# Kernel optimization log

Measured on AMD Instinct MI355X. Metric: run time of the kernel, lower is better.

Reference implementation:

```python
import jax, jax.numpy as jnp
import numpy as np

HIDDEN = 1024
NUM_HEADS = 16
HEAD_SIZE = HIDDEN // NUM_HEADS


def setup_inputs() -> dict:
    key = jax.random.key(0)
    ks = jax.random.split(key, 5)
    B, S = 2, 2048
    x = jax.random.normal(ks[0], (B, S, HIDDEN), dtype=jnp.float32)
    # nn.Linear(hidden, 3*hidden): weight stored (in, out) for x @ W
    scale_qkv = 1.0 / np.sqrt(HIDDEN)
    w_qkv = jax.random.uniform(ks[1], (HIDDEN, 3 * HIDDEN), minval=-scale_qkv, maxval=scale_qkv, dtype=jnp.float32)
    b_qkv = jax.random.uniform(ks[2], (3 * HIDDEN,), minval=-scale_qkv, maxval=scale_qkv, dtype=jnp.float32)
    w_o = jax.random.uniform(ks[3], (HIDDEN, HIDDEN), minval=-scale_qkv, maxval=scale_qkv, dtype=jnp.float32)
    b_o = jax.random.uniform(ks[4], (HIDDEN,), minval=-scale_qkv, maxval=scale_qkv, dtype=jnp.float32)
    return {"x": x, "w_qkv": w_qkv, "b_qkv": b_qkv, "w_o": w_o, "b_o": b_o}


def reference(x, w_qkv, b_qkv, w_o, b_o):
    B, S, H = x.shape
    qkv = x @ w_qkv + b_qkv  # (B, S, 3H)
    q, k, v = jnp.split(qkv, 3, axis=-1)
    # (B, S, H) -> (B, nheads, S, head_size)
    def heads(t):
        return t.reshape(B, S, NUM_HEADS, HEAD_SIZE).transpose(0, 2, 1, 3)
    q, k, v = heads(q), heads(k), heads(v)
    scores = jnp.einsum('bhqd,bhkd->bhqk', q, k) / np.sqrt(HEAD_SIZE).astype(np.float32)
    causal = jnp.tril(jnp.ones((S, S), dtype=bool))  # k <= q
    scores = jnp.where(causal, scores, -jnp.inf)
    probs = jax.nn.softmax(scores, axis=-1)
    out = jnp.einsum('bhqk,bhkd->bqhd', probs, v).reshape(B, S, H)
    return out @ w_o + b_o
```

## Files before the change

### kernel.cpp

```cpp
#include <hip/hip_runtime.h>
#include <stdint.h>


typedef __bf16 bf16;
typedef __attribute__((ext_vector_type(8))) __bf16 bf16x8;
typedef __attribute__((ext_vector_type(4))) __bf16 bf16x4;
typedef __attribute__((ext_vector_type(4))) float floatx4;

#define SCL 0.18033688011112042f

__device__ __forceinline__ floatx4 mfma_bf16(bf16x8 a, bf16x8 b, floatx4 c) {
  return __builtin_amdgcn_mfma_f32_16x16x32_bf16(a, b, c, 0, 0, 0);
}

__device__ __forceinline__ void cp_g2l_16(const bf16* g, bf16* l) {
  __builtin_amdgcn_global_load_lds(
      (const __attribute__((address_space(1))) void*)g,
      (__attribute__((address_space(3))) void*)l, 16, 0, 0);
}

__global__ __launch_bounds__(256) void prep_kernel(
    const float* __restrict__ x, bf16* __restrict__ xb,
    const float* __restrict__ w_qkv, bf16* __restrict__ wqkvt,
    const float* __restrict__ w_o, bf16* __restrict__ wot) {
  const int b = blockIdx.x;
  const int tid = threadIdx.x;
  if (b < 4096) {
    const int i = (b * 256 + tid) * 4;
    floatx4 v = *(const floatx4*)(x + i);
    bf16x4 o;
    o[0] = (bf16)v[0]; o[1] = (bf16)v[1]; o[2] = (bf16)v[2]; o[3] = (bf16)v[3];
    *(bf16x4*)(xb + i) = o;
    return;
  }
  __shared__ float tile[32][33];
  const float* W; bf16* Wt; int K, N, n0, k0;
  if (b < 7168) {
    const int bb = b - 4096;
    W = w_qkv; Wt = wqkvt; K = 1024; N = 3072;
    n0 = (bb % 96) * 32; k0 = (bb / 96) * 32;
  } else {
    const int bb = b - 7168;
    W = w_o; Wt = wot; K = 1024; N = 1024;
    n0 = (bb & 31) * 32; k0 = (bb >> 5) * 32;
  }
  const int tx = tid & 31, ty = tid >> 5;
  for (int i = 0; i < 4; ++i)
    tile[ty + 8 * i][tx] = W[(size_t)(k0 + ty + 8 * i) * N + n0 + tx];
  __syncthreads();
  for (int i = 0; i < 4; ++i)
    Wt[(size_t)(n0 + ty + 8 * i) * K + k0 + tx] = (bf16)tile[tx][ty + 8 * i];
}

template <int MODE, int MI>
__global__ __launch_bounds__(256, 3) void gemm_bt_kernel(
    const bf16* __restrict__ A, const bf16* __restrict__ Bt,
    const float* __restrict__ bias, float* __restrict__ outF,
    bf16* __restrict__ qb, bf16* __restrict__ kb, bf16* __restrict__ vtb,
    int N, int K) {
  constexpr int BM = MI * 32;
  __shared__ bf16 As[BM * 32];
  __shared__ bf16 Bs[128 * 32];
  const int tid = threadIdx.x;
  const int w = tid >> 6, lane = tid & 63;
  const int l16 = lane & 15, quad = lane >> 4;
  const int m0 = blockIdx.y * BM, n0 = blockIdx.x * 128;
  const int wm = (w & 1) * (BM / 2), wn = (w >> 1) * 64;

  const int arow = w * (BM / 4) + (lane >> 2);
  const int acol = (lane & 3) * 8;
  const bf16* Ag = A + (size_t)(m0 + arow) * K + acol;
  bf16* Al = As + arow * 32 + acol;
  const int brow = w * 32 + (lane >> 2);
  const bf16* Bg = Bt + (size_t)(n0 + brow) * K + acol;
  bf16* Bl = Bs + brow * 32 + acol;

  floatx4 acc[MI][4];
#pragma unroll
  for (int i = 0; i < MI; ++i)
#pragma unroll
    for (int j = 0; j < 4; ++j) acc[i][j] = (floatx4){0.f, 0.f, 0.f, 0.f};

  for (int k0 = 0; k0 < K; k0 += 32) {
    __syncthreads();
    cp_g2l_16(Ag + k0, Al);
    if (MI == 4) cp_g2l_16(Ag + (size_t)16 * K + k0, Al + 16 * 32);
    cp_g2l_16(Bg + k0, Bl);
    cp_g2l_16(Bg + (size_t)16 * K + k0, Bl + 16 * 32);
    __syncthreads();
    bf16x8 af[MI], bfr[4];
#pragma unroll
    for (int i = 0; i < MI; ++i)
      af[i] = *(const bf16x8*)(&As[(wm + i * 16 + l16) * 32 + quad * 8]);
#pragma unroll
    for (int j = 0; j < 4; ++j)
      bfr[j] = *(const bf16x8*)(&Bs[(wn + j * 16 + l16) * 32 + quad * 8]);
#pragma unroll
    for (int i = 0; i < MI; ++i)
#pragma unroll
      for (int j = 0; j < 4; ++j)
        acc[i][j] = mfma_bf16(af[i], bfr[j], acc[i][j]);
  }

#pragma unroll
  for (int i = 0; i < MI; ++i)
#pragma unroll
    for (int j = 0; j < 4; ++j) {
      const int nn = n0 + wn + j * 16 + l16;
      const float bv = bias[nn];
      const int mbase = m0 + wm + i * 16 + quad * 4;
      if (MODE == 1) {
#pragma unroll
        for (int r = 0; r < 4; ++r)
          outF[(size_t)(mbase + r) * N + nn] = acc[i][j][r] + bv;
      } else {
        const int which = nn >> 10;
        const int rem = nn & 1023;
        const int h = rem >> 6, d = rem & 63;
        const int b = mbase >> 11, s = mbase & 2047;
        const size_t bh = (size_t)(b * 16 + h);
        if (which == 2) {
          bf16x4 pk;
#pragma unroll
          for (int r = 0; r < 4; ++r) pk[r] = (bf16)(acc[i][j][r] + bv);
          *(bf16x4*)(vtb + (bh * 64 + d) * 2048 + s) = pk;
        } else if (which == 0) {
#pragma unroll
          for (int r = 0; r < 4; ++r)
            qb[(bh * 2048 + s + r) * 64 + d] = (bf16)((acc[i][j][r] + bv) * SCL);
        } else {
#pragma unroll
          for (int r = 0; r < 4; ++r)
            kb[(bh * 2048 + s + r) * 64 + d] = (bf16)(acc[i][j][r] + bv);
        }
      }
    }
}

__global__ __launch_bounds__(512, 4) void attn_kernel(
    const bf16* __restrict__ Qb, const bf16* __restrict__ Kb,
    const bf16* __restrict__ Vtb, bf16* __restrict__ attnb) {
  __shared__ bf16 Ks[2][4096];
  __shared__ bf16 Vs[2][4096];
  __shared__ bf16 Ps[8 * 1152];
  const int bid = blockIdx.x;
  const int bh = (bid & 7) * 4 + ((bid >> 3) & 3);
  const int p = bid >> 5;
  const int tid = threadIdx.x;
  const int w = tid >> 6, lane = tid & 63;
  const int l16 = lane & 15, quad = lane >> 4;
  const int g = (w < 4) ? p : (31 - p);
  const int q0 = g * 64 + (w & 3) * 16;
  const int b = bh >> 4, h = bh & 15;
  const bf16* Qh = Qb + (size_t)bh * 2048 * 64;
  const bf16* Kh = Kb + (size_t)bh * 2048 * 64;
  const bf16* Vh = Vtb + (size_t)bh * 64 * 2048;
  bf16* Pw = Ps + w * 1152;

  const int nt = 32 - p;
  const int wdiag = g;

  const int srow = tid >> 3;
  const int ssl = ((tid & 7) - srow) & 7;
  const int ksrc = srow * 64 + ssl * 8;
  const int vsrc = srow * 2048 + ssl * 8;

  bf16x8 qf[2];
#pragma unroll
  for (int kq = 0; kq < 2; ++kq)
    qf[kq] = *(const bf16x8*)(Qh + (size_t)(q0 + l16) * 64 + kq * 32 + quad * 8);
  bf16x8 ones;
#pragma unroll
  for (int j = 0; j < 8; ++j) ones[j] = (bf16)1.0f;

  floatx4 O[4], Ol;
#pragma unroll
  for (int nd = 0; nd < 4; ++nd) O[nd] = (floatx4){0.f, 0.f, 0.f, 0.f};
  Ol = (floatx4){0.f, 0.f, 0.f, 0.f};

  cp_g2l_16(Kh + ksrc, &Ks[0][tid * 8]);
  cp_g2l_16(Vh + vsrc, &Vs[0][tid * 8]);

  int cur = 0;
  for (int t = 0; t < nt; ++t, cur ^= 1) {
    __syncthreads();
    if (t + 1 < nt) {
      const int nb = cur ^ 1;
      cp_g2l_16(Kh + (size_t)(t + 1) * 4096 + ksrc, &Ks[nb][tid * 8]);
      cp_g2l_16(Vh + (t + 1) * 64 + vsrc, &Vs[nb][tid * 8]);
    }

    if (t > wdiag) continue;
    const bool diag = (t == wdiag);
    const bf16* KsC = Ks[cur];
    const bf16* VsC = Vs[cur];

    bf16x8 kf[4][2];
#pragma unroll
    for (int nk = 0; nk < 4; ++nk)
#pragma unroll
      for (int kq = 0; kq < 2; ++kq) {
        const int row = nk * 16 + l16;
        kf[nk][kq] = *(const bf16x8*)(
            &KsC[row * 64 + ((kq * 4 + quad + row) & 7) * 8]);
      }

    floatx4 sf[4];
#pragma unroll
    for (int nk = 0; nk < 4; ++nk) {
      floatx4 a = (floatx4){0.f, 0.f, 0.f, 0.f};
      a = mfma_bf16(kf[nk][0], qf[0], a);
      a = mfma_bf16(kf[nk][1], qf[1], a);
      sf[nk] = a;
    }

    bf16x8 vf[4][2];
#pragma unroll
    for (int nd = 0; nd < 4; ++nd)
#pragma unroll
      for (int kq = 0; kq < 2; ++kq) {
        const int row = nd * 16 + l16;
        vf[nd][kq] = *(const bf16x8*)(
            &VsC[row * 64 + ((kq * 4 + quad + row) & 7) * 8]);
      }

#pragma unroll
    for (int nk = 0; nk < 4; ++nk) {
      bf16x4 pk;
#pragma unroll
      for (int r = 0; r < 4; ++r) {
        float s = sf[nk][r];
        if (diag) {
          const int kc = t * 64 + nk * 16 + quad * 4 + r;
          const int qrow = q0 + l16;
          s = (kc <= qrow) ? s : -1e30f;
        }
        pk[r] = (bf16)__builtin_amdgcn_exp2f(s);
      }
      *(bf16x4*)(&Pw[l16 * 72 + nk * 16 + quad * 4]) = pk;
    }

    bf16x8 pf[2];
    pf[0] = *(const bf16x8*)(&Pw[l16 * 72 + quad * 8]);
    pf[1] = *(const bf16x8*)(&Pw[l16 * 72 + 32 + quad * 8]);

#pragma unroll
    for (int nd = 0; nd < 4; ++nd) {
      floatx4 o = O[nd];
      o = mfma_bf16(pf[0], vf[nd][0], o);
      o = mfma_bf16(pf[1], vf[nd][1], o);
      O[nd] = o;
    }
    Ol = mfma_bf16(pf[0], ones, Ol);
    Ol = mfma_bf16(pf[1], ones, Ol);
  }

#pragma unroll
  for (int r = 0; r < 4; ++r) {
    const int qrow = q0 + quad * 4 + r;
    const float inv = 1.f / Ol[r];
#pragma unroll
    for (int nd = 0; nd < 4; ++nd)
      attnb[((size_t)(b * 2048 + qrow)) * 1024 + h * 64 + nd * 16 + l16] =
          (bf16)(O[nd][r] * inv);
  }
}

extern "C" void kernel_launch(void* const* d_in, const int* in_sizes, int n_in,
                              void* d_out, int out_size, void* d_ws, size_t ws_size,
                              hipStream_t stream) {
  const float* x     = (const float*)d_in[0];
  const float* w_qkv = (const float*)d_in[1];
  const float* b_qkv = (const float*)d_in[2];
  const float* w_o   = (const float*)d_in[3];
  const float* b_o   = (const float*)d_in[4];
  float* out = (float*)d_out;

  char* ws = (char*)d_ws;
  bf16* xb    = (bf16*)ws; ws += (size_t)4096 * 1024 * 2;
  bf16* wqkvt = (bf16*)ws; ws += (size_t)3072 * 1024 * 2;
  bf16* wot   = (bf16*)ws; ws += (size_t)1024 * 1024 * 2;
  bf16* qb    = (bf16*)ws; ws += (size_t)32 * 2048 * 64 * 2;
  bf16* kb    = (bf16*)ws; ws += (size_t)32 * 2048 * 64 * 2;
  bf16* vtb   = (bf16*)ws; ws += (size_t)32 * 2048 * 64 * 2;
  bf16* attnb = (bf16*)ws; ws += (size_t)4096 * 1024 * 2;

  prep_kernel<<<8192, 256, 0, stream>>>(x, xb, w_qkv, wqkvt, w_o, wot);
  gemm_bt_kernel<0, 4><<<dim3(24, 32), 256, 0, stream>>>(
      xb, wqkvt, b_qkv, nullptr, qb, kb, vtb, 3072, 1024);
  attn_kernel<<<512, 512, 0, stream>>>(qb, kb, vtb, attnb);
  gemm_bt_kernel<1, 2><<<dim3(8, 64), 256, 0, stream>>>(
      attnb, wot, b_o, out, nullptr, nullptr, nullptr, 1024, 1024);
}
```

Before: 177.0 us.

## Rewrite attention with 32x32 MFMA tiles, 4 waves, split-K balanced work

The attention kernel moves from 8 waves doing 16x16x32 MFMAs over 16-row query strips to 4 waves doing 32x32x16 MFMAs over 32-row strips. Within each key tile, the two waves pairs divide the key columns, and partial O and row-sum results are reduced through shared memory at the end. This aims for more work per wave, fewer LDS fragment loads per FLOP, and better load balance between the paired causal query blocks. The cost is a larger accumulator footprint per wave (lower occupancy of 3 per CU), an extra shared-memory reduction step, and more complex control flow.

```diff
diff --git a/kernel.cpp b/kernel.cpp
--- a/kernel.cpp
+++ b/kernel.cpp
@@ -6,17 +6,29 @@
 typedef __attribute__((ext_vector_type(8))) __bf16 bf16x8;
 typedef __attribute__((ext_vector_type(4))) __bf16 bf16x4;
 typedef __attribute__((ext_vector_type(4))) float floatx4;
+typedef __attribute__((ext_vector_type(16))) float floatx16;
 
 #define SCL 0.18033688011112042f
 
 __device__ __forceinline__ floatx4 mfma_bf16(bf16x8 a, bf16x8 b, floatx4 c) {
   return __builtin_amdgcn_mfma_f32_16x16x32_bf16(a, b, c, 0, 0, 0);
+}
+
+__device__ __forceinline__ floatx16 mfma32(bf16x8 a, bf16x8 b, floatx16 c) {
+  return __builtin_amdgcn_mfma_f32_32x32x16_bf16(a, b, c, 0, 0, 0);
 }
 
 __device__ __forceinline__ void cp_g2l_16(const bf16* g, bf16* l) {
   __builtin_amdgcn_global_load_lds(
       (const __attribute__((address_space(1))) void*)g,
       (__attribute__((address_space(3))) void*)l, 16, 0, 0);
+}
+
+__device__ __forceinline__ floatx16 zero16() {
+  floatx16 z;
+#pragma unroll
+  for (int i = 0; i < 16; ++i) z[i] = 0.f;
+  return z;
 }
 
 __global__ __launch_bounds__(256) void prep_kernel(
@@ -137,132 +149,170 @@
     }
 }
 
-__global__ __launch_bounds__(512, 4) void attn_kernel(
+__global__ __launch_bounds__(256, 3) void attn_kernel(
     const bf16* __restrict__ Qb, const bf16* __restrict__ Kb,
     const bf16* __restrict__ Vtb, bf16* __restrict__ attnb) {
   __shared__ bf16 Ks[2][4096];
   __shared__ bf16 Vs[2][4096];
-  __shared__ bf16 Ps[8 * 1152];
+  __shared__ bf16 Ps[4 * 2304];
   const int bid = blockIdx.x;
   const int bh = (bid & 7) * 4 + ((bid >> 3) & 3);
   const int p = bid >> 5;
   const int tid = threadIdx.x;
   const int w = tid >> 6, lane = tid & 63;
-  const int l16 = lane & 15, quad = lane >> 4;
-  const int g = (w < 4) ? p : (31 - p);
-  const int q0 = g * 64 + (w & 3) * 16;
+  const int l31 = lane & 31, hi = lane >> 5;
   const int b = bh >> 4, h = bh & 15;
+  const bool hw = (w < 2);
+  const int gB = 31 - p;
+  const int q0A = p * 64 + (w & 1) * 32;
+  const int q0B = gB * 64 + (w & 1) * 32;
+  const int nt = 32 - p;
+
   const bf16* Qh = Qb + (size_t)bh * 2048 * 64;
   const bf16* Kh = Kb + (size_t)bh * 2048 * 64;
   const bf16* Vh = Vtb + (size_t)bh * 64 * 2048;
-  bf16* Pw = Ps + w * 1152;
-
-  const int nt = 32 - p;
-  const int wdiag = g;
-
-  const int srow = tid >> 3;
-  const int ssl = ((tid & 7) - srow) & 7;
-  const int ksrc = srow * 64 + ssl * 8;
-  const int vsrc = srow * 2048 + ssl * 8;
-
-  bf16x8 qf[2];
-#pragma unroll
-  for (int kq = 0; kq < 2; ++kq)
-    qf[kq] = *(const bf16x8*)(Qh + (size_t)(q0 + l16) * 64 + kq * 32 + quad * 8);
+  bf16* Pw = Ps + w * 2304;
+
+  const int c0 = tid, c1 = tid + 256;
+  const int kof0 = (c0 >> 3) * 64 + ((((c0 & 7) - (c0 >> 3)) & 7) * 8);
+  const int kof1 = (c1 >> 3) * 64 + ((((c1 & 7) - (c1 >> 3)) & 7) * 8);
+  const int vof0 = (c0 >> 3) * 2048 + ((((c0 & 7) - (c0 >> 3)) & 7) * 8);
+  const int vof1 = (c1 >> 3) * 2048 + ((((c1 & 7) - (c1 >> 3)) & 7) * 8);
+
+  int q0 = hw ? q0A : q0B;
+  int wdiag = hw ? p : gB;
+  bf16x8 qf[4];
+  {
+    const bf16* Qr = Qh + (size_t)(q0 + l31) * 64 + hi * 8;
+#pragma unroll
+    for (int kd = 0; kd < 4; ++kd) qf[kd] = *(const bf16x8*)(Qr + kd * 16);
+  }
   bf16x8 ones;
 #pragma unroll
   for (int j = 0; j < 8; ++j) ones[j] = (bf16)1.0f;
 
-  floatx4 O[4], Ol;
-#pragma unroll
-  for (int nd = 0; nd < 4; ++nd) O[nd] = (floatx4){0.f, 0.f, 0.f, 0.f};
-  Ol = (floatx4){0.f, 0.f, 0.f, 0.f};
-
-  cp_g2l_16(Kh + ksrc, &Ks[0][tid * 8]);
-  cp_g2l_16(Vh + vsrc, &Vs[0][tid * 8]);
+  floatx16 O0 = zero16(), O1 = zero16(), Ol = zero16();
+
+  auto do_ms = [&](int ms, const bf16* KsC, int t, bool diag, int q0c) {
+    floatx16 sf = zero16();
+    const int row = ms * 32 + l31;
+#pragma unroll
+    for (int kd = 0; kd < 4; ++kd) {
+      bf16x8 kf = *(const bf16x8*)(
+          &KsC[row * 64 + (((kd * 2 + hi) + row) & 7) * 8]);
+      sf = mfma32(kf, qf[kd], sf);
+    }
+#pragma unroll
+    for (int a = 0; a < 4; ++a) {
+      bf16x4 pk;
+#pragma unroll
+      for (int bq = 0; bq < 4; ++bq) {
+        float s = sf[a * 4 + bq];
+        if (diag) {
+          const int kc = t * 64 + ms * 32 + bq + 8 * a + 4 * hi;
+          s = (kc <= q0c + l31) ? s : -1e30f;
+        }
+        pk[bq] = (bf16)__builtin_amdgcn_exp2f(s);
+      }
+      *(bf16x4*)(&Pw[l31 * 72 + ms * 32 + 8 * a + 4 * hi]) = pk;
+    }
+  };
+
+  auto ld_p = [&](int ks) {
+    return *(const bf16x8*)(&Pw[l31 * 72 + ks * 16 + hi * 8]);
+  };
+
+  auto pv_ks = [&](const bf16* VsC, bf16x8 pfk, int ks) {
+    const int r0 = l31, r1 = 32 + l31;
+    bf16x8 v0 = *(const bf16x8*)(
+        &VsC[r0 * 64 + (((ks * 2 + hi) + r0) & 7) * 8]);
+    O0 = mfma32(pfk, v0, O0);
+    bf16x8 v1 = *(const bf16x8*)(
+        &VsC[r1 * 64 + (((ks * 2 + hi) + r1) & 7) * 8]);
+    O1 = mfma32(pfk, v1, O1);
+    Ol = mfma32(pfk, ones, Ol);
+  };
+
+  auto outW = [&](int qb) {
+#pragma unroll
+    for (int r = 0; r < 16; ++r) {
+      const int q = qb + (r & 3) + 8 * (r >> 2) + 4 * hi;
+      const float inv = 1.f / Ol[r];
+      bf16* dst = attnb + ((size_t)(b * 2048 + q)) * 1024 + h * 64;
+      dst[l31] = (bf16)(O0[r] * inv);
+      dst[32 + l31] = (bf16)(O1[r] * inv);
+    }
+  };
+
+  cp_g2l_16(Kh + kof0, &Ks[0][c0 * 8]);
+  cp_g2l_16(Kh + kof1, &Ks[0][c1 * 8]);
+  cp_g2l_16(Vh + vof0, &Vs[0][c0 * 8]);
+  cp_g2l_16(Vh + vof1, &Vs[0][c1 * 8]);
 
   int cur = 0;
   for (int t = 0; t < nt; ++t, cur ^= 1) {
     __syncthreads();
     if (t + 1 < nt) {
       const int nb = cur ^ 1;
-      cp_g2l_16(Kh + (size_t)(t + 1) * 4096 + ksrc, &Ks[nb][tid * 8]);
-      cp_g2l_16(Vh + (t + 1) * 64 + vsrc, &Vs[nb][tid * 8]);
-    }
-
-    if (t > wdiag) continue;
-    const bool diag = (t == wdiag);
+      cp_g2l_16(Kh + (size_t)(t + 1) * 4096 + kof0, &Ks[nb][c0 * 8]);
+      cp_g2l_16(Kh + (size_t)(t + 1) * 4096 + kof1, &Ks[nb][c1 * 8]);
+      cp_g2l_16(Vh + (size_t)(t + 1) * 64 + vof0, &Vs[nb][c0 * 8]);
+      cp_g2l_16(Vh + (size_t)(t + 1) * 64 + vof1, &Vs[nb][c1 * 8]);
+    }
     const bf16* KsC = Ks[cur];
     const bf16* VsC = Vs[cur];
-
-    bf16x8 kf[4][2];
-#pragma unroll
-    for (int nk = 0; nk < 4; ++nk)
-#pragma unroll
-      for (int kq = 0; kq < 2; ++kq) {
-        const int row = nk * 16 + l16;
-        kf[nk][kq] = *(const bf16x8*)(
-            &KsC[row * 64 + ((kq * 4 + quad + row) & 7) * 8]);
-      }
-
-    floatx4 sf[4];
-#pragma unroll
-    for (int nk = 0; nk < 4; ++nk) {
-      floatx4 a = (floatx4){0.f, 0.f, 0.f, 0.f};
-      a = mfma_bf16(kf[nk][0], qf[0], a);
-      a = mfma_bf16(kf[nk][1], qf[1], a);
-      sf[nk] = a;
-    }
-
-    bf16x8 vf[4][2];
-#pragma unroll
-    for (int nd = 0; nd < 4; ++nd)
-#pragma unroll
-      for (int kq = 0; kq < 2; ++kq) {
-        const int row = nd * 16 + l16;
-        vf[nd][kq] = *(const bf16x8*)(
-            &VsC[row * 64 + ((kq * 4 + quad + row) & 7) * 8]);
-      }
-
-#pragma unroll
-    for (int nk = 0; nk < 4; ++nk) {
-      bf16x4 pk;
-#pragma unroll
-      for (int r = 0; r < 4; ++r) {
-        float s = sf[nk][r];
-        if (diag) {
-          const int kc = t * 64 + nk * 16 + quad * 4 + r;
-          const int qrow = q0 + l16;
-          s = (kc <= qrow) ? s : -1e30f;
-        }
-        pk[r] = (bf16)__builtin_amdgcn_exp2f(s);
-      }
-      *(bf16x4*)(&Pw[l16 * 72 + nk * 16 + quad * 4]) = pk;
-    }
-
-    bf16x8 pf[2];
-    pf[0] = *(const bf16x8*)(&Pw[l16 * 72 + quad * 8]);
-    pf[1] = *(const bf16x8*)(&Pw[l16 * 72 + 32 + quad * 8]);
-
-#pragma unroll
-    for (int nd = 0; nd < 4; ++nd) {
-      floatx4 o = O[nd];
-      o = mfma_bf16(pf[0], vf[nd][0], o);
-      o = mfma_bf16(pf[1], vf[nd][1], o);
-      O[nd] = o;
-    }
-    Ol = mfma_bf16(pf[0], ones, Ol);
-    Ol = mfma_bf16(pf[1], ones, Ol);
-  }
-
-#pragma unroll
-  for (int r = 0; r < 4; ++r) {
-    const int qrow = q0 + quad * 4 + r;
-    const float inv = 1.f / Ol[r];
-#pragma unroll
-    for (int nd = 0; nd < 4; ++nd)
-      attnb[((size_t)(b * 2048 + qrow)) * 1024 + h * 64 + nd * 16 + l16] =
-          (bf16)(O[nd][r] * inv);
+    const bool full = (t <= p);
+    const bool diag = (t == wdiag);
+
+    if (full) {
+      do_ms(0, KsC, t, diag, q0);
+      do_ms(1, KsC, t, diag, q0);
+      bf16x8 p0 = ld_p(0), p1 = ld_p(1), p2 = ld_p(2), p3 = ld_p(3);
+      pv_ks(VsC, p0, 0); pv_ks(VsC, p1, 1);
+      pv_ks(VsC, p2, 2); pv_ks(VsC, p3, 3);
+    } else if (hw) {
+      do_ms(1, KsC, t, diag, q0);
+      bf16x8 p2 = ld_p(2), p3 = ld_p(3);
+      pv_ks(VsC, p2, 2); pv_ks(VsC, p3, 3);
+    } else {
+      do_ms(0, KsC, t, diag, q0);
+      bf16x8 p0 = ld_p(0), p1 = ld_p(1);
+      pv_ks(VsC, p0, 0); pv_ks(VsC, p1, 1);
+    }
+
+    if (hw && t == p) {
+      outW(q0A);
+      O0 = zero16(); O1 = zero16(); Ol = zero16();
+      q0 = q0B; wdiag = gB;
+      const bf16* Qr = Qh + (size_t)(q0B + l31) * 64 + hi * 8;
+#pragma unroll
+      for (int kd = 0; kd < 4; ++kd) qf[kd] = *(const bf16x8*)(Qr + kd * 16);
+    }
+  }
+
+  __syncthreads();
+  float* sO = (float*)(&Vs[0][0]);
+  float* sL = (float*)(&Ks[0][0]);
+  if (hw) {
+#pragma unroll
+    for (int r = 0; r < 16; ++r) {
+      const int ql = (r & 3) + 8 * (r >> 2) + 4 * hi;
+      sO[w * 2048 + ql * 64 + l31] = O0[r];
+      sO[w * 2048 + ql * 64 + 32 + l31] = O1[r];
+      if (l31 == 0) sL[w * 32 + ql] = Ol[r];
+    }
+  }
+  __syncthreads();
+  if (!hw) {
+    const int pw = w - 2;
+#pragma unroll
+    for (int r = 0; r < 16; ++r) {
+      const int ql = (r & 3) + 8 * (r >> 2) + 4 * hi;
+      O0[r] += sO[pw * 2048 + ql * 64 + l31];
+      O1[r] += sO[pw * 2048 + ql * 64 + 32 + l31];
+      Ol[r] += sL[pw * 32 + ql];
+    }
+    outW(q0B);
   }
 }
 
@@ -288,7 +338,7 @@
   prep_kernel<<<8192, 256, 0, stream>>>(x, xb, w_qkv, wqkvt, w_o, wot);
   gemm_bt_kernel<0, 4><<<dim3(24, 32), 256, 0, stream>>>(
       xb, wqkvt, b_qkv, nullptr, qb, kb, vtb, 3072, 1024);
-  attn_kernel<<<512, 512, 0, stream>>>(qb, kb, vtb, attnb);
+  attn_kernel<<<512, 256, 0, stream>>>(qb, kb, vtb, attnb);
   gemm_bt_kernel<1, 2><<<dim3(8, 64), 256, 0, stream>>>(
       attnb, wot, b_o, out, nullptr, nullptr, nullptr, 1024, 1024);
 }
```

Result: slower. 198.8 us (+12.3%).
